# Performance work log

Measured on AMD Instinct MI355X. Metric: run time of the kernel, lower is better.

Reference implementation:

```python
import jax, jax.numpy as jnp
import numpy as np

B, T, V, L = 131072, 6, 31, 3  # batch, seq_len, vocab/hidden, num RNN layers


def setup_inputs() -> dict:
    key = jax.random.key(0)
    ks = jax.random.split(key, 8)
    s = 1.0 / np.sqrt(V)  # torch default init scale for RNN/Linear
    return {
        "inp": jax.random.normal(ks[0], (B, T, V), dtype=jnp.float32),
        "h0": jax.random.normal(ks[1], (L, B, V), dtype=jnp.float32),
        "W_ih": jax.random.uniform(ks[2], (L, V, V), jnp.float32, -s, s),
        "W_hh": jax.random.uniform(ks[3], (L, V, V), jnp.float32, -s, s),
        "b_ih": jax.random.uniform(ks[4], (L, V), jnp.float32, -s, s),
        "b_hh": jax.random.uniform(ks[5], (L, V), jnp.float32, -s, s),
        "W_lin": jax.random.uniform(ks[6], (V, V), jnp.float32, -s, s),
        "b_lin": jax.random.uniform(ks[7], (V,), jnp.float32, -s, s),
    }


def _rnn_layer(x_tm, h0_l, wih, whh, bih, bhh):
    # x_tm: [T, B, V] time-major; h0_l: [B, V]
    def step(h, x_t):
        h_new = jnp.tanh(x_t @ wih.T + bih + h @ whh.T + bhh)
        return h_new, h_new

    _, ys = jax.lax.scan(step, h0_l, x_tm)
    return ys  # [T, B, V]


def reference(inp, h0, W_ih, W_hh, b_ih, b_hh, W_lin, b_lin):
    x = jnp.transpose(inp, (1, 0, 2))  # [T, B, V] time-major
    for l in range(L):
        x = _rnn_layer(x, h0[l], W_ih[l], W_hh[l], b_ih[l], b_hh[l])
    y = jnp.tanh(x @ W_lin.T + b_lin)  # [T, B, V]
    last = y[-1]  # [B, V] == y[:, -1, :] in batch-major
    return jax.nn.softmax(last, axis=1)
```

## Files before the change

### kernel.cpp

```cpp
#include <hip/hip_runtime.h>
#include <hip/hip_bf16.h>


#define VD 31
#define TD 6
#define SCL 2.8853900817779268f

typedef __attribute__((ext_vector_type(8))) short bf16x8;
typedef __attribute__((ext_vector_type(4))) float f32x4;
typedef __attribute__((ext_vector_type(4))) unsigned u32x4;
typedef float f32x4u __attribute__((ext_vector_type(4), aligned(4)));

struct raw8 { f32x4u a, b; };

__device__ __forceinline__ short f2bf(float f) {
    unsigned u = __float_as_uint(f);
    unsigned r = (u + 0x7fffu + ((u >> 16) & 1u)) >> 16;
    return (short)r;
}

__device__ __forceinline__ unsigned f2bf2u(float lo, float hi) {
    union { __hip_bfloat162 h2; unsigned u; } cvt;
    cvt.h2 = __float22bfloat162_rn(make_float2(lo, hi));
    return cvt.u;
}

__device__ __forceinline__ float fexp2(float x) {
#if __has_builtin(__builtin_amdgcn_exp2f)
    return __builtin_amdgcn_exp2f(x);
#else
    float r; asm("v_exp_f32 %0, %1" : "=v"(r) : "v"(x)); return r;
#endif
}

__device__ __forceinline__ float tanh_pre(float c) {
    float e = fexp2(c);
    float r = __builtin_amdgcn_rcpf(e + 1.0f);
    return __builtin_fmaf(-2.0f, r, 1.0f);
}

__device__ __forceinline__ raw8 load_raw(const float* __restrict__ p, int fo) {
    raw8 r;
    r.a = *(const f32x4u*)(p + fo);
    r.b = *(const f32x4u*)(p + fo + 4);
    return r;
}

__device__ __forceinline__ bf16x8 cvt_frag(raw8 r, bool q3) {
    float l[8] = {r.a[0], r.a[1], r.a[2], r.a[3], r.b[0], r.b[1], r.b[2], r.b[3]};
    float s[8];
#pragma unroll
    for (int j = 0; j < 7; ++j) s[j] = q3 ? l[j + 1] : l[j];
    s[7] = q3 ? 1.0f : l[7];
    union { u32x4 u4; bf16x8 b8; } cvt;
#pragma unroll
    for (int j = 0; j < 4; ++j) cvt.u4[j] = f2bf2u(s[2 * j], s[2 * j + 1]);
    return cvt.b8;
}

__device__ __forceinline__ bf16x8 load_wfrag(const float* __restrict__ W,
                                             const float* __restrict__ b1,
                                             const float* __restrict__ b2,
                                             int i, int half, int k0) {
    const int nn = 8 * (i >> 2) + (i & 3) + 4 * half;
    bf16x8 r;
#pragma unroll
    for (int j = 0; j < 8; ++j) {
        int k = k0 + j;
        float v = 0.0f;
        if (nn < VD) {
            if (k < VD) v = W[nn * VD + k];
            else v = (b1 ? b1[nn] : 0.0f) + (b2 ? b2[nn] : 0.0f);
        }
        r[j] = f2bf(v * SCL);
    }
    return r;
}

__device__ __forceinline__ bf16x8 layer_step(bf16x8 x, bf16x8 h,
    bf16x8 wi0, bf16x8 wi1, bf16x8 wh0, bf16x8 wh1, bool q3)
{
    const f32x4 z = {0.0f, 0.0f, 0.0f, 0.0f};
    f32x4 c0 = __builtin_amdgcn_mfma_f32_16x16x32_bf16(wh0, h, z, 0, 0, 0);
    f32x4 c1 = __builtin_amdgcn_mfma_f32_16x16x32_bf16(wh1, h, z, 0, 0, 0);
    c0 = __builtin_amdgcn_mfma_f32_16x16x32_bf16(wi0, x, c0, 0, 0, 0);
    c1 = __builtin_amdgcn_mfma_f32_16x16x32_bf16(wi1, x, c1, 0, 0, 0);
    float t0 = tanh_pre(c0[0]), t1 = tanh_pre(c0[1]);
    float t2 = tanh_pre(c0[2]), t3 = tanh_pre(c0[3]);
    float t4 = tanh_pre(c1[0]), t5 = tanh_pre(c1[1]);
    float t6 = tanh_pre(c1[2]);
    float t7 = q3 ? 1.0f : tanh_pre(c1[3]);
    union { u32x4 u4; bf16x8 b8; } cvt;
    cvt.u4[0] = f2bf2u(t0, t1);
    cvt.u4[1] = f2bf2u(t2, t3);
    cvt.u4[2] = f2bf2u(t4, t5);
    cvt.u4[3] = f2bf2u(t6, t7);
    return cvt.b8;
}

__global__ __launch_bounds__(256, 1) void rnn_mfma(
    const float* __restrict__ inp,
    const float* __restrict__ h0,
    const float* __restrict__ Wih,
    const float* __restrict__ Whh,
    const float* __restrict__ bih,
    const float* __restrict__ bhh,
    const float* __restrict__ Wlin,
    const float* __restrict__ blin,
    float* __restrict__ out,
    int B)
{
    const int wave = threadIdx.x >> 6;
    const int lane = threadIdx.x & 63;
    const int cb   = lane & 15;
    const int quad = lane >> 4;
    const int k0   = quad * 8;
    const bool q3  = (quad == 3);
    const int fo   = q3 ? 23 : k0;
    const int bbase = (blockIdx.x * 4 + wave) * 32;
    if (bbase >= B) return;

    const float* W0 = Wih;               const float* U0 = Whh;
    const float* W1 = Wih + VD * VD;     const float* U1 = Whh + VD * VD;
    const float* W2 = Wih + 2 * VD * VD; const float* U2 = Whh + 2 * VD * VD;
    const bf16x8 wiA0 = load_wfrag(W0, bih, bhh, cb, 0, k0);
    const bf16x8 wiA1 = load_wfrag(W0, bih, bhh, cb, 1, k0);
    const bf16x8 whA0 = load_wfrag(U0, nullptr, nullptr, cb, 0, k0);
    const bf16x8 whA1 = load_wfrag(U0, nullptr, nullptr, cb, 1, k0);
    const bf16x8 wiB0 = load_wfrag(W1, bih + VD, bhh + VD, cb, 0, k0);
    const bf16x8 wiB1 = load_wfrag(W1, bih + VD, bhh + VD, cb, 1, k0);
    const bf16x8 whB0 = load_wfrag(U1, nullptr, nullptr, cb, 0, k0);
    const bf16x8 whB1 = load_wfrag(U1, nullptr, nullptr, cb, 1, k0);
    const bf16x8 wiC0 = load_wfrag(W2, bih + 2 * VD, bhh + 2 * VD, cb, 0, k0);
    const bf16x8 wiC1 = load_wfrag(W2, bih + 2 * VD, bhh + 2 * VD, cb, 1, k0);
    const bf16x8 whC0 = load_wfrag(U2, nullptr, nullptr, cb, 0, k0);
    const bf16x8 whC1 = load_wfrag(U2, nullptr, nullptr, cb, 1, k0);
    const bf16x8 wl0  = load_wfrag(Wlin, blin, nullptr, cb, 0, k0);
    const bf16x8 wl1  = load_wfrag(Wlin, blin, nullptr, cb, 1, k0);

    bf16x8 h1a = cvt_frag(load_raw(h0 + ((size_t)0 * B + bbase + cb) * VD, fo), q3);
    bf16x8 h1b = cvt_frag(load_raw(h0 + ((size_t)0 * B + bbase + 16 + cb) * VD, fo), q3);
    bf16x8 h2a = cvt_frag(load_raw(h0 + ((size_t)1 * B + bbase + cb) * VD, fo), q3);
    bf16x8 h2b = cvt_frag(load_raw(h0 + ((size_t)1 * B + bbase + 16 + cb) * VD, fo), q3);
    bf16x8 h3a = cvt_frag(load_raw(h0 + ((size_t)2 * B + bbase + cb) * VD, fo), q3);
    bf16x8 h3b = cvt_frag(load_raw(h0 + ((size_t)2 * B + bbase + 16 + cb) * VD, fo), q3);

    const float* xrow0 = inp + (size_t)(bbase + cb) * TD * VD;
    const float* xrow1 = inp + (size_t)(bbase + 16 + cb) * TD * VD;

    raw8 rx0 = load_raw(xrow0, fo);
    raw8 rx1 = load_raw(xrow1, fo);

#pragma unroll
    for (int v = 0; v < TD + 2; ++v) {
        if (v >= 2) {
            h3a = layer_step(h2a, h3a, wiC0, wiC1, whC0, whC1, q3);
            h3b = layer_step(h2b, h3b, wiC0, wiC1, whC0, whC1, q3);
        }
        if (v >= 1 && v < TD + 1) {
            h2a = layer_step(h1a, h2a, wiB0, wiB1, whB0, whB1, q3);
            h2b = layer_step(h1b, h2b, wiB0, wiB1, whB0, whB1, q3);
        }
        if (v < TD) {
            bf16x8 ax0 = cvt_frag(rx0, q3);
            bf16x8 ax1 = cvt_frag(rx1, q3);
            if (v + 1 < TD) {
                rx0 = load_raw(xrow0 + (v + 1) * VD, fo);
                rx1 = load_raw(xrow1 + (v + 1) * VD, fo);
            }
            h1a = layer_step(ax0, h1a, wiA0, wiA1, whA0, whA1, q3);
            h1b = layer_step(ax1, h1b, wiA0, wiA1, whA0, whA1, q3);
        }
    }

    const f32x4 z = {0.0f, 0.0f, 0.0f, 0.0f};
#pragma unroll
    for (int tb = 0; tb < 2; ++tb) {
        bf16x8 h3 = tb ? h3b : h3a;
        f32x4 c0 = __builtin_amdgcn_mfma_f32_16x16x32_bf16(wl0, h3, z, 0, 0, 0);
        f32x4 c1 = __builtin_amdgcn_mfma_f32_16x16x32_bf16(wl1, h3, z, 0, 0, 0);
        float v0 = tanh_pre(c0[0]), v1 = tanh_pre(c0[1]);
        float v2 = tanh_pre(c0[2]), v3 = tanh_pre(c0[3]);
        float v4 = tanh_pre(c1[0]), v5 = tanh_pre(c1[1]);
        float v6 = tanh_pre(c1[2]), v7 = tanh_pre(c1[3]);
        float mx = fmaxf(fmaxf(fmaxf(v0, v1), fmaxf(v2, v3)),
                         fmaxf(fmaxf(v4, v5), fmaxf(v6, v7)));
        mx = fmaxf(mx, __shfl_xor(mx, 16));
        mx = fmaxf(mx, __shfl_xor(mx, 32));
        float e0 = __expf(v0 - mx), e1 = __expf(v1 - mx);
        float e2 = __expf(v2 - mx), e3 = __expf(v3 - mx);
        float e4 = __expf(v4 - mx), e5 = __expf(v5 - mx);
        float e6 = __expf(v6 - mx);
        float e7 = q3 ? 0.0f : __expf(v7 - mx);
        float s = ((e0 + e1) + (e2 + e3)) + ((e4 + e5) + (e6 + e7));
        s += __shfl_xor(s, 16);
        s += __shfl_xor(s, 32);
        const float inv = __builtin_amdgcn_rcpf(s);
        const size_t row = (size_t)(bbase + tb * 16 + cb);
        float* po = out + row * VD + k0;
        f32x4u lo = {e0 * inv, e1 * inv, e2 * inv, e3 * inv};
        *(f32x4u*)po = lo;
        if (!q3) {
            f32x4u hi = {e4 * inv, e5 * inv, e6 * inv, e7 * inv};
            *(f32x4u*)(po + 4) = hi;
        } else {
            po[4] = e4 * inv;
            po[5] = e5 * inv;
            po[6] = e6 * inv;
        }
    }
}

extern "C" void kernel_launch(void* const* d_in, const int* in_sizes, int n_in,
                              void* d_out, int out_size, void* d_ws, size_t ws_size,
                              hipStream_t stream) {
    const float* inp  = (const float*)d_in[0];
    const float* h0   = (const float*)d_in[1];
    const float* Wih  = (const float*)d_in[2];
    const float* Whh  = (const float*)d_in[3];
    const float* bih  = (const float*)d_in[4];
    const float* bhh  = (const float*)d_in[5];
    const float* Wlin = (const float*)d_in[6];
    const float* blin = (const float*)d_in[7];
    float* out = (float*)d_out;

    const int B = in_sizes[0] / (TD * VD);
    const int grid = (B + 127) / 128;
    rnn_mfma<<<grid, 256, 0, stream>>>(inp, h0, Wih, Whh, bih, bhh, Wlin, blin, out, B);
}
```

Baseline: 227.3 us.

## Stage weights in LDS and replace wavefront layer schedule with sequential per-step loop

All RNN and linear weights and biases are first copied cooperatively into shared memory by the block, and each wave builds its bf16 MFMA fragments from LDS instead of issuing scattered global loads per lane. The time loop also drops the skewed wavefront schedule across the three layers in favour of a plain, non-unrolled loop that runs layers 1-3 in order each step. This reduces redundant global weight traffic, but adds a block barrier and removes the independent work that let the MFMAs of different layers interleave, which lengthens the dependency chain per step.

```diff
diff --git a/kernel.cpp b/kernel.cpp
--- a/kernel.cpp
+++ b/kernel.cpp
@@ -5,6 +5,14 @@
 #define VD 31
 #define TD 6
 #define SCL 2.8853900817779268f
+
+#define WIH_OFF  0
+#define WHH_OFF  2883
+#define WLIN_OFF 5766
+#define BIH_OFF  6727
+#define BHH_OFF  6820
+#define BLIN_OFF 6913
+#define WTOT     6944
 
 typedef __attribute__((ext_vector_type(8))) short bf16x8;
 typedef __attribute__((ext_vector_type(4))) float f32x4;
@@ -58,9 +66,8 @@
     return cvt.b8;
 }
 
-__device__ __forceinline__ bf16x8 load_wfrag(const float* __restrict__ W,
-                                             const float* __restrict__ b1,
-                                             const float* __restrict__ b2,
+__device__ __forceinline__ bf16x8 load_wfrag(const float* lds, int woff,
+                                             int b1off, int b2off,
                                              int i, int half, int k0) {
     const int nn = 8 * (i >> 2) + (i & 3) + 4 * half;
     bf16x8 r;
@@ -69,8 +76,11 @@
         int k = k0 + j;
         float v = 0.0f;
         if (nn < VD) {
-            if (k < VD) v = W[nn * VD + k];
-            else v = (b1 ? b1[nn] : 0.0f) + (b2 ? b2[nn] : 0.0f);
+            if (k < VD) v = lds[woff + nn * VD + k];
+            else {
+                if (b1off >= 0) v += lds[b1off + nn];
+                if (b2off >= 0) v += lds[b2off + nn];
+            }
         }
         r[j] = f2bf(v * SCL);
     }
@@ -110,33 +120,46 @@
     float* __restrict__ out,
     int B)
 {
-    const int wave = threadIdx.x >> 6;
-    const int lane = threadIdx.x & 63;
+    __shared__ __align__(16) float warena[WTOT];
+
+    const int tid  = threadIdx.x;
+    const int wave = tid >> 6;
+    const int lane = tid & 63;
     const int cb   = lane & 15;
     const int quad = lane >> 4;
     const int k0   = quad * 8;
     const bool q3  = (quad == 3);
     const int fo   = q3 ? 23 : k0;
     const int bbase = (blockIdx.x * 4 + wave) * 32;
+
+    for (int i = tid; i < 3 * VD * VD; i += 256) {
+        warena[WIH_OFF + i] = Wih[i];
+        warena[WHH_OFF + i] = Whh[i];
+    }
+    for (int i = tid; i < VD * VD; i += 256) warena[WLIN_OFF + i] = Wlin[i];
+    if (tid < 3 * VD) {
+        warena[BIH_OFF + tid] = bih[tid];
+        warena[BHH_OFF + tid] = bhh[tid];
+    }
+    if (tid < VD) warena[BLIN_OFF + tid] = blin[tid];
+    __syncthreads();
+
     if (bbase >= B) return;
 
-    const float* W0 = Wih;               const float* U0 = Whh;
-    const float* W1 = Wih + VD * VD;     const float* U1 = Whh + VD * VD;
-    const float* W2 = Wih + 2 * VD * VD; const float* U2 = Whh + 2 * VD * VD;
-    const bf16x8 wiA0 = load_wfrag(W0, bih, bhh, cb, 0, k0);
-    const bf16x8 wiA1 = load_wfrag(W0, bih, bhh, cb, 1, k0);
-    const bf16x8 whA0 = load_wfrag(U0, nullptr, nullptr, cb, 0, k0);
-    const bf16x8 whA1 = load_wfrag(U0, nullptr, nullptr, cb, 1, k0);
-    const bf16x8 wiB0 = load_wfrag(W1, bih + VD, bhh + VD, cb, 0, k0);
-    const bf16x8 wiB1 = load_wfrag(W1, bih + VD, bhh + VD, cb, 1, k0);
-    const bf16x8 whB0 = load_wfrag(U1, nullptr, nullptr, cb, 0, k0);
-    const bf16x8 whB1 = load_wfrag(U1, nullptr, nullptr, cb, 1, k0);
-    const bf16x8 wiC0 = load_wfrag(W2, bih + 2 * VD, bhh + 2 * VD, cb, 0, k0);
-    const bf16x8 wiC1 = load_wfrag(W2, bih + 2 * VD, bhh + 2 * VD, cb, 1, k0);
-    const bf16x8 whC0 = load_wfrag(U2, nullptr, nullptr, cb, 0, k0);
-    const bf16x8 whC1 = load_wfrag(U2, nullptr, nullptr, cb, 1, k0);
-    const bf16x8 wl0  = load_wfrag(Wlin, blin, nullptr, cb, 0, k0);
-    const bf16x8 wl1  = load_wfrag(Wlin, blin, nullptr, cb, 1, k0);
+    const bf16x8 wiA0 = load_wfrag(warena, WIH_OFF,          BIH_OFF,          BHH_OFF,          cb, 0, k0);
+    const bf16x8 wiA1 = load_wfrag(warena, WIH_OFF,          BIH_OFF,          BHH_OFF,          cb, 1, k0);
+    const bf16x8 whA0 = load_wfrag(warena, WHH_OFF,          -1, -1,           cb, 0, k0);
+    const bf16x8 whA1 = load_wfrag(warena, WHH_OFF,          -1, -1,           cb, 1, k0);
+    const bf16x8 wiB0 = load_wfrag(warena, WIH_OFF + VD*VD,  BIH_OFF + VD,     BHH_OFF + VD,     cb, 0, k0);
+    const bf16x8 wiB1 = load_wfrag(warena, WIH_OFF + VD*VD,  BIH_OFF + VD,     BHH_OFF + VD,     cb, 1, k0);
+    const bf16x8 whB0 = load_wfrag(warena, WHH_OFF + VD*VD,  -1, -1,           cb, 0, k0);
+    const bf16x8 whB1 = load_wfrag(warena, WHH_OFF + VD*VD,  -1, -1,           cb, 1, k0);
+    const bf16x8 wiC0 = load_wfrag(warena, WIH_OFF + 2*VD*VD, BIH_OFF + 2*VD,  BHH_OFF + 2*VD,   cb, 0, k0);
+    const bf16x8 wiC1 = load_wfrag(warena, WIH_OFF + 2*VD*VD, BIH_OFF + 2*VD,  BHH_OFF + 2*VD,   cb, 1, k0);
+    const bf16x8 whC0 = load_wfrag(warena, WHH_OFF + 2*VD*VD, -1, -1,          cb, 0, k0);
+    const bf16x8 whC1 = load_wfrag(warena, WHH_OFF + 2*VD*VD, -1, -1,          cb, 1, k0);
+    const bf16x8 wl0  = load_wfrag(warena, WLIN_OFF,         BLIN_OFF, -1,     cb, 0, k0);
+    const bf16x8 wl1  = load_wfrag(warena, WLIN_OFF,         BLIN_OFF, -1,     cb, 1, k0);
 
     bf16x8 h1a = cvt_frag(load_raw(h0 + ((size_t)0 * B + bbase + cb) * VD, fo), q3);
     bf16x8 h1b = cvt_frag(load_raw(h0 + ((size_t)0 * B + bbase + 16 + cb) * VD, fo), q3);
@@ -151,26 +174,19 @@
     raw8 rx0 = load_raw(xrow0, fo);
     raw8 rx1 = load_raw(xrow1, fo);
 
-#pragma unroll
-    for (int v = 0; v < TD + 2; ++v) {
-        if (v >= 2) {
-            h3a = layer_step(h2a, h3a, wiC0, wiC1, whC0, whC1, q3);
-            h3b = layer_step(h2b, h3b, wiC0, wiC1, whC0, whC1, q3);
+    for (int t = 0; t < TD; ++t) {
+        bf16x8 ax0 = cvt_frag(rx0, q3);
+        bf16x8 ax1 = cvt_frag(rx1, q3);
+        if (t + 1 < TD) {
+            rx0 = load_raw(xrow0 + (t + 1) * VD, fo);
+            rx1 = load_raw(xrow1 + (t + 1) * VD, fo);
         }
-        if (v >= 1 && v < TD + 1) {
-            h2a = layer_step(h1a, h2a, wiB0, wiB1, whB0, whB1, q3);
-            h2b = layer_step(h1b, h2b, wiB0, wiB1, whB0, whB1, q3);
-        }
-        if (v < TD) {
-            bf16x8 ax0 = cvt_frag(rx0, q3);
-            bf16x8 ax1 = cvt_frag(rx1, q3);
-            if (v + 1 < TD) {
-                rx0 = load_raw(xrow0 + (v + 1) * VD, fo);
-                rx1 = load_raw(xrow1 + (v + 1) * VD, fo);
-            }
-            h1a = layer_step(ax0, h1a, wiA0, wiA1, whA0, whA1, q3);
-            h1b = layer_step(ax1, h1b, wiA0, wiA1, whA0, whA1, q3);
-        }
+        h1a = layer_step(ax0, h1a, wiA0, wiA1, whA0, whA1, q3);
+        h1b = layer_step(ax1, h1b, wiA0, wiA1, whA0, whA1, q3);
+        h2a = layer_step(h1a, h2a, wiB0, wiB1, whB0, whB1, q3);
+        h2b = layer_step(h1b, h2b, wiB0, wiB1, whB0, whB1, q3);
+        h3a = layer_step(h2a, h3a, wiC0, wiC1, whC0, whC1, q3);
+        h3b = layer_step(h2b, h3b, wiC0, wiC1, whC0, whC1, q3);
     }
 
     const f32x4 z = {0.0f, 0.0f, 0.0f, 0.0f};
```

Result: faster. 218.5 us (-3.9%).

## Process four 16-row tiles per wave and drop the layer-wavefront schedule

Applied to the files above, without the earlier changes.

Each wave now handles 64 batch rows (four MFMA tiles) instead of 32, which halves the grid and amortizes the per-wave weight-fragment loads over twice as many rows. The skewed wavefront across layers is replaced by a plain, non-unrolled time loop that runs layers 1-3 in order each step. Four independent tiles per layer give the MFMA pipeline ILP in place of the cross-layer overlap. The cost is higher register pressure and half as many waves to hide memory latency, since the grid is halved.

```diff
diff --git a/kernel.cpp b/kernel.cpp
--- a/kernel.cpp
+++ b/kernel.cpp
@@ -98,6 +98,43 @@
     return cvt.b8;
 }
 
+__device__ __forceinline__ void epilogue_one(bf16x8 h3, bf16x8 wl0, bf16x8 wl1,
+                                             bool q3, int k0, size_t row,
+                                             float* __restrict__ out)
+{
+    const f32x4 z = {0.0f, 0.0f, 0.0f, 0.0f};
+    f32x4 c0 = __builtin_amdgcn_mfma_f32_16x16x32_bf16(wl0, h3, z, 0, 0, 0);
+    f32x4 c1 = __builtin_amdgcn_mfma_f32_16x16x32_bf16(wl1, h3, z, 0, 0, 0);
+    float v0 = tanh_pre(c0[0]), v1 = tanh_pre(c0[1]);
+    float v2 = tanh_pre(c0[2]), v3 = tanh_pre(c0[3]);
+    float v4 = tanh_pre(c1[0]), v5 = tanh_pre(c1[1]);
+    float v6 = tanh_pre(c1[2]), v7 = tanh_pre(c1[3]);
+    float mx = fmaxf(fmaxf(fmaxf(v0, v1), fmaxf(v2, v3)),
+                     fmaxf(fmaxf(v4, v5), fmaxf(v6, v7)));
+    mx = fmaxf(mx, __shfl_xor(mx, 16));
+    mx = fmaxf(mx, __shfl_xor(mx, 32));
+    float e0 = __expf(v0 - mx), e1 = __expf(v1 - mx);
+    float e2 = __expf(v2 - mx), e3 = __expf(v3 - mx);
+    float e4 = __expf(v4 - mx), e5 = __expf(v5 - mx);
+    float e6 = __expf(v6 - mx);
+    float e7 = q3 ? 0.0f : __expf(v7 - mx);
+    float s = ((e0 + e1) + (e2 + e3)) + ((e4 + e5) + (e6 + e7));
+    s += __shfl_xor(s, 16);
+    s += __shfl_xor(s, 32);
+    const float inv = __builtin_amdgcn_rcpf(s);
+    float* po = out + row * VD + k0;
+    f32x4u lo = {e0 * inv, e1 * inv, e2 * inv, e3 * inv};
+    *(f32x4u*)po = lo;
+    if (!q3) {
+        f32x4u hi = {e4 * inv, e5 * inv, e6 * inv, e7 * inv};
+        *(f32x4u*)(po + 4) = hi;
+    } else {
+        po[4] = e4 * inv;
+        po[5] = e5 * inv;
+        po[6] = e6 * inv;
+    }
+}
+
 __global__ __launch_bounds__(256, 1) void rnn_mfma(
     const float* __restrict__ inp,
     const float* __restrict__ h0,
@@ -117,7 +154,7 @@
     const int k0   = quad * 8;
     const bool q3  = (quad == 3);
     const int fo   = q3 ? 23 : k0;
-    const int bbase = (blockIdx.x * 4 + wave) * 32;
+    const int bbase = (blockIdx.x * 4 + wave) * 64;
     if (bbase >= B) return;
 
     const float* W0 = Wih;               const float* U0 = Whh;
@@ -138,77 +175,60 @@
     const bf16x8 wl0  = load_wfrag(Wlin, blin, nullptr, cb, 0, k0);
     const bf16x8 wl1  = load_wfrag(Wlin, blin, nullptr, cb, 1, k0);
 
-    bf16x8 h1a = cvt_frag(load_raw(h0 + ((size_t)0 * B + bbase + cb) * VD, fo), q3);
-    bf16x8 h1b = cvt_frag(load_raw(h0 + ((size_t)0 * B + bbase + 16 + cb) * VD, fo), q3);
-    bf16x8 h2a = cvt_frag(load_raw(h0 + ((size_t)1 * B + bbase + cb) * VD, fo), q3);
-    bf16x8 h2b = cvt_frag(load_raw(h0 + ((size_t)1 * B + bbase + 16 + cb) * VD, fo), q3);
-    bf16x8 h3a = cvt_frag(load_raw(h0 + ((size_t)2 * B + bbase + cb) * VD, fo), q3);
-    bf16x8 h3b = cvt_frag(load_raw(h0 + ((size_t)2 * B + bbase + 16 + cb) * VD, fo), q3);
-
-    const float* xrow0 = inp + (size_t)(bbase + cb) * TD * VD;
-    const float* xrow1 = inp + (size_t)(bbase + 16 + cb) * TD * VD;
-
-    raw8 rx0 = load_raw(xrow0, fo);
-    raw8 rx1 = load_raw(xrow1, fo);
-
-#pragma unroll
-    for (int v = 0; v < TD + 2; ++v) {
-        if (v >= 2) {
-            h3a = layer_step(h2a, h3a, wiC0, wiC1, whC0, whC1, q3);
-            h3b = layer_step(h2b, h3b, wiC0, wiC1, whC0, whC1, q3);
+    const size_t r0 = (size_t)(bbase + cb);
+    bf16x8 h1_0 = cvt_frag(load_raw(h0 + ((size_t)0 * B + r0     ) * VD, fo), q3);
+    bf16x8 h1_1 = cvt_frag(load_raw(h0 + ((size_t)0 * B + r0 + 16) * VD, fo), q3);
+    bf16x8 h1_2 = cvt_frag(load_raw(h0 + ((size_t)0 * B + r0 + 32) * VD, fo), q3);
+    bf16x8 h1_3 = cvt_frag(load_raw(h0 + ((size_t)0 * B + r0 + 48) * VD, fo), q3);
+    bf16x8 h2_0 = cvt_frag(load_raw(h0 + ((size_t)1 * B + r0     ) * VD, fo), q3);
+    bf16x8 h2_1 = cvt_frag(load_raw(h0 + ((size_t)1 * B + r0 + 16) * VD, fo), q3);
+    bf16x8 h2_2 = cvt_frag(load_raw(h0 + ((size_t)1 * B + r0 + 32) * VD, fo), q3);
+    bf16x8 h2_3 = cvt_frag(load_raw(h0 + ((size_t)1 * B + r0 + 48) * VD, fo), q3);
+    bf16x8 h3_0 = cvt_frag(load_raw(h0 + ((size_t)2 * B + r0     ) * VD, fo), q3);
+    bf16x8 h3_1 = cvt_frag(load_raw(h0 + ((size_t)2 * B + r0 + 16) * VD, fo), q3);
+    bf16x8 h3_2 = cvt_frag(load_raw(h0 + ((size_t)2 * B + r0 + 32) * VD, fo), q3);
+    bf16x8 h3_3 = cvt_frag(load_raw(h0 + ((size_t)2 * B + r0 + 48) * VD, fo), q3);
+
+    const float* xr0 = inp + (r0     ) * TD * VD;
+    const float* xr1 = inp + (r0 + 16) * TD * VD;
+    const float* xr2 = inp + (r0 + 32) * TD * VD;
+    const float* xr3 = inp + (r0 + 48) * TD * VD;
+
+    raw8 rx0 = load_raw(xr0, fo);
+    raw8 rx1 = load_raw(xr1, fo);
+    raw8 rx2 = load_raw(xr2, fo);
+    raw8 rx3 = load_raw(xr3, fo);
+
+#pragma unroll 1
+    for (int t = 0; t < TD; ++t) {
+        bf16x8 ax0 = cvt_frag(rx0, q3);
+        bf16x8 ax1 = cvt_frag(rx1, q3);
+        bf16x8 ax2 = cvt_frag(rx2, q3);
+        bf16x8 ax3 = cvt_frag(rx3, q3);
+        if (t + 1 < TD) {
+            rx0 = load_raw(xr0 + (t + 1) * VD, fo);
+            rx1 = load_raw(xr1 + (t + 1) * VD, fo);
+            rx2 = load_raw(xr2 + (t + 1) * VD, fo);
+            rx3 = load_raw(xr3 + (t + 1) * VD, fo);
         }
-        if (v >= 1 && v < TD + 1) {
-            h2a = layer_step(h1a, h2a, wiB0, wiB1, whB0, whB1, q3);
-            h2b = layer_step(h1b, h2b, wiB0, wiB1, whB0, whB1, q3);
-        }
-        if (v < TD) {
-            bf16x8 ax0 = cvt_frag(rx0, q3);
-            bf16x8 ax1 = cvt_frag(rx1, q3);
-            if (v + 1 < TD) {
-                rx0 = load_raw(xrow0 + (v + 1) * VD, fo);
-                rx1 = load_raw(xrow1 + (v + 1) * VD, fo);
-            }
-            h1a = layer_step(ax0, h1a, wiA0, wiA1, whA0, whA1, q3);
-            h1b = layer_step(ax1, h1b, wiA0, wiA1, whA0, whA1, q3);
-        }
+        h1_0 = layer_step(ax0,  h1_0, wiA0, wiA1, whA0, whA1, q3);
+        h1_1 = layer_step(ax1,  h1_1, wiA0, wiA1, whA0, whA1, q3);
+        h1_2 = layer_step(ax2,  h1_2, wiA0, wiA1, whA0, whA1, q3);
+        h1_3 = layer_step(ax3,  h1_3, wiA0, wiA1, whA0, whA1, q3);
+        h2_0 = layer_step(h1_0, h2_0, wiB0, wiB1, whB0, whB1, q3);
+        h2_1 = layer_step(h1_1, h2_1, wiB0, wiB1, whB0, whB1, q3);
+        h2_2 = layer_step(h1_2, h2_2, wiB0, wiB1, whB0, whB1, q3);
+        h2_3 = layer_step(h1_3, h2_3, wiB0, wiB1, whB0, whB1, q3);
+        h3_0 = layer_step(h2_0, h3_0, wiC0, wiC1, whC0, whC1, q3);
+        h3_1 = layer_step(h2_1, h3_1, wiC0, wiC1, whC0, whC1, q3);
+        h3_2 = layer_step(h2_2, h3_2, wiC0, wiC1, whC0, whC1, q3);
+        h3_3 = layer_step(h2_3, h3_3, wiC0, wiC1, whC0, whC1, q3);
     }
 
-    const f32x4 z = {0.0f, 0.0f, 0.0f, 0.0f};
-#pragma unroll
-    for (int tb = 0; tb < 2; ++tb) {
-        bf16x8 h3 = tb ? h3b : h3a;
-        f32x4 c0 = __builtin_amdgcn_mfma_f32_16x16x32_bf16(wl0, h3, z, 0, 0, 0);
-        f32x4 c1 = __builtin_amdgcn_mfma_f32_16x16x32_bf16(wl1, h3, z, 0, 0, 0);
-        float v0 = tanh_pre(c0[0]), v1 = tanh_pre(c0[1]);
-        float v2 = tanh_pre(c0[2]), v3 = tanh_pre(c0[3]);
-        float v4 = tanh_pre(c1[0]), v5 = tanh_pre(c1[1]);
-        float v6 = tanh_pre(c1[2]), v7 = tanh_pre(c1[3]);
-        float mx = fmaxf(fmaxf(fmaxf(v0, v1), fmaxf(v2, v3)),
-                         fmaxf(fmaxf(v4, v5), fmaxf(v6, v7)));
-        mx = fmaxf(mx, __shfl_xor(mx, 16));
-        mx = fmaxf(mx, __shfl_xor(mx, 32));
-        float e0 = __expf(v0 - mx), e1 = __expf(v1 - mx);
-        float e2 = __expf(v2 - mx), e3 = __expf(v3 - mx);
-        float e4 = __expf(v4 - mx), e5 = __expf(v5 - mx);
-        float e6 = __expf(v6 - mx);
-        float e7 = q3 ? 0.0f : __expf(v7 - mx);
-        float s = ((e0 + e1) + (e2 + e3)) + ((e4 + e5) + (e6 + e7));
-        s += __shfl_xor(s, 16);
-        s += __shfl_xor(s, 32);
-        const float inv = __builtin_amdgcn_rcpf(s);
-        const size_t row = (size_t)(bbase + tb * 16 + cb);
-        float* po = out + row * VD + k0;
-        f32x4u lo = {e0 * inv, e1 * inv, e2 * inv, e3 * inv};
-        *(f32x4u*)po = lo;
-        if (!q3) {
-            f32x4u hi = {e4 * inv, e5 * inv, e6 * inv, e7 * inv};
-            *(f32x4u*)(po + 4) = hi;
-        } else {
-            po[4] = e4 * inv;
-            po[5] = e5 * inv;
-            po[6] = e6 * inv;
-        }
-    }
+    epilogue_one(h3_0, wl0, wl1, q3, k0, r0,      out);
+    epilogue_one(h3_1, wl0, wl1, q3, k0, r0 + 16, out);
+    epilogue_one(h3_2, wl0, wl1, q3, k0, r0 + 32, out);
+    epilogue_one(h3_3, wl0, wl1, q3, k0, r0 + 48, out);
 }
 
 extern "C" void kernel_launch(void* const* d_in, const int* in_sizes, int n_in,
@@ -225,6 +245,6 @@
     float* out = (float*)d_out;
 
     const int B = in_sizes[0] / (TD * VD);
-    const int grid = (B + 127) / 128;
+    const int grid = (B + 255) / 256;
     rnn_mfma<<<grid, 256, 0, stream>>>(inp, h0, Wih, Whh, bih, bhh, Wlin, blin, out, B);
 }
```

Result: faster. 221.9 us (-2.4%).

## Stage weight fragments in LDS and shrink per-wave tile to raise occupancy

Applied to the files above, without the earlier changes.

Wave 0 of each block converts all 14 weight fragments to bf16 once and stores them in shared memory, and every wave then reads them from LDS each step instead of holding them in registers. Each wave now handles 16 batch rows instead of 32, the wavefront pipeline across layers becomes a simple unroll-1 time loop, the grid doubles, and launch bounds ask for 8 blocks per CU. The aim is to cut register pressure and raise occupancy so global-memory latency is better hidden. The cost is a block-level barrier, repeated LDS reads of the weights, and less instruction-level parallelism per wave, since the two independent row tiles and the layer skew are gone.

```diff
diff --git a/kernel.cpp b/kernel.cpp
--- a/kernel.cpp
+++ b/kernel.cpp
@@ -98,7 +98,7 @@
     return cvt.b8;
 }
 
-__global__ __launch_bounds__(256, 1) void rnn_mfma(
+__global__ __launch_bounds__(256, 8) void rnn_mfma(
     const float* __restrict__ inp,
     const float* __restrict__ h0,
     const float* __restrict__ Wih,
@@ -110,73 +110,64 @@
     float* __restrict__ out,
     int B)
 {
-    const int wave = threadIdx.x >> 6;
-    const int lane = threadIdx.x & 63;
+    __shared__ __align__(16) short wtab[14 * 512];
+
+    const int tid  = threadIdx.x;
+    const int wave = tid >> 6;
+    const int lane = tid & 63;
     const int cb   = lane & 15;
     const int quad = lane >> 4;
     const int k0   = quad * 8;
     const bool q3  = (quad == 3);
     const int fo   = q3 ? 23 : k0;
-    const int bbase = (blockIdx.x * 4 + wave) * 32;
+    const int bbase = (blockIdx.x * 4 + wave) * 16;
+
+    if (wave == 0) {
+        const float* W0 = Wih;               const float* U0 = Whh;
+        const float* W1 = Wih + VD * VD;     const float* U1 = Whh + VD * VD;
+        const float* W2 = Wih + 2 * VD * VD; const float* U2 = Whh + 2 * VD * VD;
+        short* p = wtab + lane * 8;
+        *(bf16x8*)(p + 0 * 512)  = load_wfrag(W0, bih, bhh, lane & 15, 0, k0);
+        *(bf16x8*)(p + 1 * 512)  = load_wfrag(W0, bih, bhh, lane & 15, 1, k0);
+        *(bf16x8*)(p + 2 * 512)  = load_wfrag(U0, nullptr, nullptr, lane & 15, 0, k0);
+        *(bf16x8*)(p + 3 * 512)  = load_wfrag(U0, nullptr, nullptr, lane & 15, 1, k0);
+        *(bf16x8*)(p + 4 * 512)  = load_wfrag(W1, bih + VD, bhh + VD, lane & 15, 0, k0);
+        *(bf16x8*)(p + 5 * 512)  = load_wfrag(W1, bih + VD, bhh + VD, lane & 15, 1, k0);
+        *(bf16x8*)(p + 6 * 512)  = load_wfrag(U1, nullptr, nullptr, lane & 15, 0, k0);
+        *(bf16x8*)(p + 7 * 512)  = load_wfrag(U1, nullptr, nullptr, lane & 15, 1, k0);
+        *(bf16x8*)(p + 8 * 512)  = load_wfrag(W2, bih + 2 * VD, bhh + 2 * VD, lane & 15, 0, k0);
+        *(bf16x8*)(p + 9 * 512)  = load_wfrag(W2, bih + 2 * VD, bhh + 2 * VD, lane & 15, 1, k0);
+        *(bf16x8*)(p + 10 * 512) = load_wfrag(U2, nullptr, nullptr, lane & 15, 0, k0);
+        *(bf16x8*)(p + 11 * 512) = load_wfrag(U2, nullptr, nullptr, lane & 15, 1, k0);
+        *(bf16x8*)(p + 12 * 512) = load_wfrag(Wlin, blin, nullptr, lane & 15, 0, k0);
+        *(bf16x8*)(p + 13 * 512) = load_wfrag(Wlin, blin, nullptr, lane & 15, 1, k0);
+    }
+    __syncthreads();
     if (bbase >= B) return;
 
-    const float* W0 = Wih;               const float* U0 = Whh;
-    const float* W1 = Wih + VD * VD;     const float* U1 = Whh + VD * VD;
-    const float* W2 = Wih + 2 * VD * VD; const float* U2 = Whh + 2 * VD * VD;
-    const bf16x8 wiA0 = load_wfrag(W0, bih, bhh, cb, 0, k0);
-    const bf16x8 wiA1 = load_wfrag(W0, bih, bhh, cb, 1, k0);
-    const bf16x8 whA0 = load_wfrag(U0, nullptr, nullptr, cb, 0, k0);
-    const bf16x8 whA1 = load_wfrag(U0, nullptr, nullptr, cb, 1, k0);
-    const bf16x8 wiB0 = load_wfrag(W1, bih + VD, bhh + VD, cb, 0, k0);
-    const bf16x8 wiB1 = load_wfrag(W1, bih + VD, bhh + VD, cb, 1, k0);
-    const bf16x8 whB0 = load_wfrag(U1, nullptr, nullptr, cb, 0, k0);
-    const bf16x8 whB1 = load_wfrag(U1, nullptr, nullptr, cb, 1, k0);
-    const bf16x8 wiC0 = load_wfrag(W2, bih + 2 * VD, bhh + 2 * VD, cb, 0, k0);
-    const bf16x8 wiC1 = load_wfrag(W2, bih + 2 * VD, bhh + 2 * VD, cb, 1, k0);
-    const bf16x8 whC0 = load_wfrag(U2, nullptr, nullptr, cb, 0, k0);
-    const bf16x8 whC1 = load_wfrag(U2, nullptr, nullptr, cb, 1, k0);
-    const bf16x8 wl0  = load_wfrag(Wlin, blin, nullptr, cb, 0, k0);
-    const bf16x8 wl1  = load_wfrag(Wlin, blin, nullptr, cb, 1, k0);
-
-    bf16x8 h1a = cvt_frag(load_raw(h0 + ((size_t)0 * B + bbase + cb) * VD, fo), q3);
-    bf16x8 h1b = cvt_frag(load_raw(h0 + ((size_t)0 * B + bbase + 16 + cb) * VD, fo), q3);
-    bf16x8 h2a = cvt_frag(load_raw(h0 + ((size_t)1 * B + bbase + cb) * VD, fo), q3);
-    bf16x8 h2b = cvt_frag(load_raw(h0 + ((size_t)1 * B + bbase + 16 + cb) * VD, fo), q3);
-    bf16x8 h3a = cvt_frag(load_raw(h0 + ((size_t)2 * B + bbase + cb) * VD, fo), q3);
-    bf16x8 h3b = cvt_frag(load_raw(h0 + ((size_t)2 * B + bbase + 16 + cb) * VD, fo), q3);
-
-    const float* xrow0 = inp + (size_t)(bbase + cb) * TD * VD;
-    const float* xrow1 = inp + (size_t)(bbase + 16 + cb) * TD * VD;
-
-    raw8 rx0 = load_raw(xrow0, fo);
-    raw8 rx1 = load_raw(xrow1, fo);
-
-#pragma unroll
-    for (int v = 0; v < TD + 2; ++v) {
-        if (v >= 2) {
-            h3a = layer_step(h2a, h3a, wiC0, wiC1, whC0, whC1, q3);
-            h3b = layer_step(h2b, h3b, wiC0, wiC1, whC0, whC1, q3);
-        }
-        if (v >= 1 && v < TD + 1) {
-            h2a = layer_step(h1a, h2a, wiB0, wiB1, whB0, whB1, q3);
-            h2b = layer_step(h1b, h2b, wiB0, wiB1, whB0, whB1, q3);
-        }
-        if (v < TD) {
-            bf16x8 ax0 = cvt_frag(rx0, q3);
-            bf16x8 ax1 = cvt_frag(rx1, q3);
-            if (v + 1 < TD) {
-                rx0 = load_raw(xrow0 + (v + 1) * VD, fo);
-                rx1 = load_raw(xrow1 + (v + 1) * VD, fo);
-            }
-            h1a = layer_step(ax0, h1a, wiA0, wiA1, whA0, whA1, q3);
-            h1b = layer_step(ax1, h1b, wiA0, wiA1, whA0, whA1, q3);
-        }
-    }
-
-    const f32x4 z = {0.0f, 0.0f, 0.0f, 0.0f};
-#pragma unroll
-    for (int tb = 0; tb < 2; ++tb) {
-        bf16x8 h3 = tb ? h3b : h3a;
+    const short* tp = wtab + lane * 8;
+#define LDF(f) (*(const bf16x8*)(tp + (f) * 512))
+
+    bf16x8 h1 = cvt_frag(load_raw(h0 + ((size_t)0 * B + bbase + cb) * VD, fo), q3);
+    bf16x8 h2 = cvt_frag(load_raw(h0 + ((size_t)1 * B + bbase + cb) * VD, fo), q3);
+    bf16x8 h3 = cvt_frag(load_raw(h0 + ((size_t)2 * B + bbase + cb) * VD, fo), q3);
+
+    const float* xrow = inp + (size_t)(bbase + cb) * TD * VD;
+    raw8 rx = load_raw(xrow, fo);
+
+#pragma unroll 1
+    for (int t = 0; t < TD; ++t) {
+        bf16x8 ax = cvt_frag(rx, q3);
+        if (t + 1 < TD)
+            rx = load_raw(xrow + (t + 1) * VD, fo);
+        h1 = layer_step(ax, h1, LDF(0), LDF(1), LDF(2),  LDF(3),  q3);
+        h2 = layer_step(h1, h2, LDF(4), LDF(5), LDF(6),  LDF(7),  q3);
+        h3 = layer_step(h2, h3, LDF(8), LDF(9), LDF(10), LDF(11), q3);
+    }
+
+    {
+        const f32x4 z = {0.0f, 0.0f, 0.0f, 0.0f};
+        bf16x8 wl0 = LDF(12), wl1 = LDF(13);
         f32x4 c0 = __builtin_amdgcn_mfma_f32_16x16x32_bf16(wl0, h3, z, 0, 0, 0);
         f32x4 c1 = __builtin_amdgcn_mfma_f32_16x16x32_bf16(wl1, h3, z, 0, 0, 0);
         float v0 = tanh_pre(c0[0]), v1 = tanh_pre(c0[1]);
@@ -196,7 +187,7 @@
         s += __shfl_xor(s, 16);
         s += __shfl_xor(s, 32);
         const float inv = __builtin_amdgcn_rcpf(s);
-        const size_t row = (size_t)(bbase + tb * 16 + cb);
+        const size_t row = (size_t)(bbase + cb);
         float* po = out + row * VD + k0;
         f32x4u lo = {e0 * inv, e1 * inv, e2 * inv, e3 * inv};
         *(f32x4u*)po = lo;
@@ -209,6 +200,7 @@
             po[6] = e6 * inv;
         }
     }
+#undef LDF
 }
 
 extern "C" void kernel_launch(void* const* d_in, const int* in_sizes, int n_in,
@@ -225,6 +217,6 @@
     float* out = (float*)d_out;
 
     const int B = in_sizes[0] / (TD * VD);
-    const int grid = (B + 127) / 128;
+    const int grid = (B + 63) / 64;
     rnn_mfma<<<grid, 256, 0, stream>>>(inp, h0, Wih, Whh, bih, bhh, Wlin, blin, out, B);
 }
```

New measurement: 252.2 us. 11.0% more time.
